# Optimization experiments

Measured on AMD Instinct MI355X. Metric: run time of the kernel, lower is better.

The kernel has to match this reference:

```python
import jax, jax.numpy as jnp
import numpy as np

HEADS = 4
DIM_HEAD = 32
SCALE = DIM_HEAD ** -0.5

# Energy conventions (Hopfield / Lagrangian formulation):
#  Neuron(x): g = activation(x); e = sum(x*g) - L(x)
#  Synapse(g, x): e = -sum(g*x)
#  identity Lagrangian: L(x) = 0.5*sum(x^2), g = x  => Conv2d block energy = -0.5*sum(x^2)
#  softmax Lagrangian: L(x) = sum(logsumexp(x, -1)), g = softmax(x, -1)

def setup_inputs() -> dict:
    key = jax.random.key(0)
    ks = jax.random.split(key, 5)
    b, c, h, w = 8, 256, 48, 48
    hidden = HEADS * DIM_HEAD  # 128
    return {
        "x": jax.random.normal(ks[0], (b, c, h, w), jnp.float32),
        "w_qkv": jax.random.normal(ks[1], (hidden * 3, c), jnp.float32) * 0.02,
        "b_qkv": jax.random.normal(ks[2], (hidden * 3,), jnp.float32) * 0.02,
        "w_out": jax.random.normal(ks[3], (c, hidden), jnp.float32) * 0.02,
        "b_out": jax.random.normal(ks[4], (c,), jnp.float32) * 0.02,
    }

def reference(x, w_qkv, b_qkv, w_out, b_out):
    b, c, h, w = x.shape
    # 1x1 conv == channel matmul
    qkv = jnp.einsum('oc,bcxy->boxy', w_qkv, x) + b_qkv[None, :, None, None]
    e_qkv = -0.5 * jnp.sum(qkv * qkv)  # identity-Lagrangian neuron + synapse energy
    q, k, v = jnp.split(qkv, 3, axis=1)
    # 'b (h c) x y -> b h c (x y)'
    def heads(t):
        return t.reshape(b, HEADS, DIM_HEAD, h * w)
    q, k, v = heads(q), heads(k), heads(v)
    q = q * SCALE
    sim = jnp.einsum('bhdi,bhdj->bhij', q, k)  # [b, heads, hw, hw]
    sim = sim - jax.lax.stop_gradient(jnp.max(sim, axis=-1, keepdims=True))
    attn = jax.nn.softmax(sim, axis=-1)
    # softmax-Lagrangian neuron energy: sum(sim*attn) - sum(logsumexp(sim, -1))
    e_attn = jnp.sum(sim * attn) - jnp.sum(jax.nn.logsumexp(sim, axis=-1))
    out = jnp.einsum('bhij,bhdj->bhid', attn, v)  # [b, heads, hw, dim_head]
    # 'b h (x y) d -> b (h d) x y'
    out = out.transpose(0, 1, 3, 2).reshape(b, HEADS * DIM_HEAD, h, w)
    out = jnp.einsum('oc,bcxy->boxy', w_out, out) + b_out[None, :, None, None]
    e_out = -0.5 * jnp.sum(out * out)
    return out, e_attn + e_out + e_qkv
```

## Files before the change

### kernel.cpp

```cpp
#include <hip/hip_runtime.h>
#include <hip/hip_bf16.h>

#define HW 2304
#define NB 8
#define NC 256
#define HID 128
#define DH 32
#define NH 4
#define SCALE 0.17677669529663687f
#define LOG2E 1.4426950408889634f
#define LN2   0.6931471805599453f

using bf16x8 = __attribute__((ext_vector_type(8))) short;
using f32x4  = __attribute__((ext_vector_type(4))) float;

__device__ __forceinline__ short f2bf(float f) {
    unsigned u = __float_as_uint(f);
    u += 0x7FFF + ((u >> 16) & 1);
    return (short)(u >> 16);
}
__device__ __forceinline__ unsigned pk2bf(float a, float b) {
    union { __hip_bfloat162 h; unsigned u; } cv;
    cv.h = __float22bfloat162_rn(float2{a, b});
    return cv.u;
}
__device__ __forceinline__ void gld16(const void* g, void* l) {
    __builtin_amdgcn_global_load_lds(
        (const __attribute__((address_space(1))) unsigned*)g,
        (__attribute__((address_space(3))) unsigned*)l, 16, 0, 0);
}

__global__ __launch_bounds__(256)
void prep(const float* __restrict__ x, const float* __restrict__ wq,
          const float* __restrict__ wo, short* __restrict__ Xt,
          short* __restrict__ Wq, short* __restrict__ Wo, float* __restrict__ wsz)
{
    if (blockIdx.z == 8) {
        const int bid = blockIdx.x + 72 * blockIdx.y;
        if (bid == 0 && threadIdx.x == 0) { wsz[0] = 0.f; ((int*)wsz)[1] = 0; }
        const int i = bid * 256 + threadIdx.x;
        if (i < 384 * 256) Wq[i] = f2bf(wq[i]);
        if (i < 256 * 128) Wo[i] = f2bf(wo[i]);
        return;
    }
    __shared__ float T[32][33];
    const int b = blockIdx.z, c0 = blockIdx.y * 32, s0 = blockIdx.x * 32;
    const int ts = threadIdx.x & 31, tc = threadIdx.x >> 5;
    #pragma unroll
    for (int cc = tc; cc < 32; cc += 8)
        T[cc][ts] = x[((size_t)b * NC + c0 + cc) * HW + s0 + ts];
    __syncthreads();
    const int tcc = threadIdx.x & 31, tss = threadIdx.x >> 5;
    #pragma unroll
    for (int ss = tss; ss < 32; ss += 8)
        Xt[((size_t)b * HW + s0 + ss) * NC + c0 + tcc] = f2bf(T[tcc][ss]);
}

template<int KD, bool QKV>
__global__ __launch_bounds__(256, 4)
void conv_mfma(const short* __restrict__ A, const short* __restrict__ Bt,
               const float* __restrict__ bias, float* __restrict__ out0,
               short* __restrict__ Qb, short* __restrict__ Kb,
               short* __restrict__ Vb, float* __restrict__ E,
               int* __restrict__ ticket, int nblocks, float* __restrict__ edst)
{
    const int b  = blockIdx.z;
    const int bm = blockIdx.y * 64;
    const int bn = blockIdx.x * 128;
    const int t  = threadIdx.x;
    const int w  = t >> 6, lane = t & 63;
    const int n16 = lane & 15, quad = lane >> 4;

    __shared__ __align__(16) char csm[24576];
    __shared__ float red[4];

    const int rL = lane >> 2, cswz = (lane & 3) ^ (rL & 3);
    const char* agl = (const char*)(A  + (size_t)(bm + rL) * KD + cswz * 8);
    const char* bgl = (const char*)(Bt + ((size_t)b * HW + bn + rL) * KD + cswz * 8);

    auto issue = [&](int kc, int pbuf) {
        char* base = csm + pbuf * 12288;
        if (w == 0) {
            gld16(agl + (size_t)(0 * 16 * KD + kc) * 2, base + 0 * 1024);
            gld16(agl + (size_t)(1 * 16 * KD + kc) * 2, base + 1 * 1024);
            gld16(bgl + (size_t)(0 * 16 * KD + kc) * 2, base + 4096 + 0 * 1024);
        } else if (w == 1) {
            gld16(agl + (size_t)(2 * 16 * KD + kc) * 2, base + 2 * 1024);
            gld16(agl + (size_t)(3 * 16 * KD + kc) * 2, base + 3 * 1024);
            gld16(bgl + (size_t)(1 * 16 * KD + kc) * 2, base + 4096 + 1 * 1024);
        } else if (w == 2) {
            gld16(bgl + (size_t)(2 * 16 * KD + kc) * 2, base + 4096 + 2 * 1024);
            gld16(bgl + (size_t)(3 * 16 * KD + kc) * 2, base + 4096 + 3 * 1024);
            gld16(bgl + (size_t)(4 * 16 * KD + kc) * 2, base + 4096 + 4 * 1024);
        } else {
            gld16(bgl + (size_t)(5 * 16 * KD + kc) * 2, base + 4096 + 5 * 1024);
            gld16(bgl + (size_t)(6 * 16 * KD + kc) * 2, base + 4096 + 6 * 1024);
            gld16(bgl + (size_t)(7 * 16 * KD + kc) * 2, base + 4096 + 7 * 1024);
        }
    };

    f32x4 acc[4][2] = {};
    const int rsw = (quad ^ (n16 & 3)) * 16;
    constexpr int NI = KD / 32;

    issue(0, 0);
    for (int ki = 0; ki < NI; ++ki) {
        const int p = ki & 1;
        __syncthreads();
        if (ki + 1 < NI) issue((ki + 1) * 32, p ^ 1);

        const char* Ap = csm + p * 12288;
        const char* Bp = Ap + 4096;
        bf16x8 am[4], bq[2];
        #pragma unroll
        for (int tm = 0; tm < 4; ++tm)
            am[tm] = *(const bf16x8*)(Ap + tm * 1024 + n16 * 64 + rsw);
        #pragma unroll
        for (int j = 0; j < 2; ++j)
            bq[j] = *(const bf16x8*)(Bp + (w * 2 + j) * 1024 + n16 * 64 + rsw);
        #pragma unroll
        for (int tm = 0; tm < 4; ++tm)
            #pragma unroll
            for (int j = 0; j < 2; ++j)
                acc[tm][j] = __builtin_amdgcn_mfma_f32_16x16x32_bf16(am[tm], bq[j], acc[tm][j], 0, 0, 0);
    }

    float e = 0.f;
    #pragma unroll
    for (int tm = 0; tm < 4; ++tm) {
        const int o0 = bm + tm * 16 + quad * 4;
        const float4 bb = *(const float4*)(bias + o0);
        #pragma unroll
        for (int j = 0; j < 2; ++j) {
            const int s = bn + (w * 2 + j) * 16 + n16;
            float v[4] = {acc[tm][j][0] + bb.x, acc[tm][j][1] + bb.y,
                          acc[tm][j][2] + bb.z, acc[tm][j][3] + bb.w};
            e -= 0.5f * (v[0]*v[0] + v[1]*v[1] + v[2]*v[2] + v[3]*v[3]);
            if (QKV) {
                if (o0 < HID) {
                    const int h = o0 >> 5, dh0 = o0 & 31;
                    const float qs = SCALE * LOG2E;
                    short4 pk = {f2bf(v[0]*qs), f2bf(v[1]*qs),
                                 f2bf(v[2]*qs), f2bf(v[3]*qs)};
                    *(short4*)(Qb + ((size_t)(b * NH + h) * HW + s) * DH + dh0) = pk;
                } else if (o0 < 2 * HID) {
                    const int c = o0 - HID, h = c >> 5, dh0 = c & 31;
                    const int g = s & 31;
                    const int sp = (s & ~31) | ((g & 4) << 2) | ((g >> 3) << 2) | (g & 3);
                    short4 pk = {f2bf(v[0]), f2bf(v[1]), f2bf(v[2]), f2bf(v[3])};
                    *(short4*)(Kb + ((size_t)(b * NH + h) * HW + sp) * DH + dh0) = pk;
                } else {
                    const int c = o0 - 2 * HID, h = c >> 5, dh0 = c & 31;
                    #pragma unroll
                    for (int r = 0; r < 4; ++r)
                        Vb[((size_t)(b * NH + h) * DH + dh0 + r) * HW + s] = f2bf(v[r]);
                }
            } else {
                #pragma unroll
                for (int r = 0; r < 4; ++r)
                    out0[((size_t)b * NC + o0 + r) * HW + s] = v[r];
            }
        }
    }

    #pragma unroll
    for (int off = 32; off > 0; off >>= 1) e += __shfl_down(e, off);
    if (lane == 0) red[w] = e;
    __syncthreads();
    if (t == 0) {
        atomicAdd(E, red[0] + red[1] + red[2] + red[3]);
        if (!QKV) {
            __threadfence();
            const int prev = atomicAdd(ticket, 1);
            if (prev == nblocks - 1) {
                __threadfence();
                edst[0] = atomicAdd(E, 0.f);
            }
        }
    }
}

__global__ __launch_bounds__(256)
void flash9(const short* __restrict__ Qb, const short* __restrict__ Kb,
            const short* __restrict__ Vb, short* __restrict__ attT,
            float* __restrict__ E)
{
    __shared__ __align__(16) char smem[16384];

    const int bh   = blockIdx.y;
    const int w    = threadIdx.x >> 6;
    const int lane = threadIdx.x & 63;
    const int n16  = lane & 15, quad = lane >> 4;
    const int qb   = blockIdx.x * 128 + w * 32;

    bf16x8 aq[2];
    #pragma unroll
    for (int qg = 0; qg < 2; ++qg)
        aq[qg] = *(const bf16x8*)(Qb + ((size_t)bh * HW + qb + qg * 16 + n16) * DH + quad * 8);

    const int rL = lane >> 2, cL = (lane & 3) ^ (rL & 3);
    const char* gbase; size_t gstep;
    if (w < 2) {
        gbase = (const char*)(Kb + (size_t)bh * HW * DH) + ((w & 1) * 16 + rL) * 64 + cL * 16;
        gstep = 2048;
    } else {
        gbase = (const char*)(Vb + (size_t)bh * DH * HW)
              + (size_t)((w & 1) * 16 + rL) * (HW * 2) + cL * 16;
        gstep = 64;
    }

    gld16(gbase,         smem + 0    + w * 1024);
    gld16(gbase + gstep, smem + 4096 + w * 1024);

    f32x4 acc[2][2] = {};
    float ls[2] = {}, ts[2] = {};
    const int swz = (quad ^ (n16 & 3)) * 8;

    for (int it = 0; it < 36; ++it) {
        const int p = it & 1;
        __syncthreads();
        if (it + 1 < 36) {
            const size_t g0 = (size_t)(2 * it + 2) * gstep;
            gld16(gbase + g0,         smem + (p ^ 1) * 8192 + 0    + w * 1024);
            gld16(gbase + g0 + gstep, smem + (p ^ 1) * 8192 + 4096 + w * 1024);
        }

        #pragma unroll
        for (int ca = 0; ca < 2; ++ca) {
            const short* kb = (const short*)(smem + p * 8192 + ca * 4096);

            const bf16x8 bk0 = *(const bf16x8*)(kb + n16 * 32 + swz);
            const bf16x8 bk1 = *(const bf16x8*)(kb + 512  + n16 * 32 + swz);
            const bf16x8 bv0 = *(const bf16x8*)(kb + 1024 + n16 * 32 + swz);
            const bf16x8 bv1 = *(const bf16x8*)(kb + 1536 + n16 * 32 + swz);

            #pragma unroll
            for (int qg = 0; qg < 2; ++qg) {
                f32x4 z = {};
                const f32x4 s0 = __builtin_amdgcn_mfma_f32_16x16x32_bf16(bk0, aq[qg], z, 0, 0, 0);
                const f32x4 s1 = __builtin_amdgcn_mfma_f32_16x16x32_bf16(bk1, aq[qg], z, 0, 0, 0);
                float e0[4], e1[4];
                #pragma unroll
                for (int r = 0; r < 4; ++r) {
                    e0[r] = __builtin_amdgcn_exp2f(s0[r]);
                    e1[r] = __builtin_amdgcn_exp2f(s1[r]);
                }
                ls[qg] += (e0[0] + e0[1]) + (e0[2] + e0[3])
                        + (e1[0] + e1[1]) + (e1[2] + e1[3]);
                ts[qg] += (e0[0]*s0[0] + e0[1]*s0[1]) + (e0[2]*s0[2] + e0[3]*s0[3])
                        + (e1[0]*s1[0] + e1[1]*s1[1]) + (e1[2]*s1[2] + e1[3]*s1[3]);
                union { bf16x8 v; unsigned u[4]; } pa;
                pa.u[0] = pk2bf(e0[0], e0[1]);
                pa.u[1] = pk2bf(e0[2], e0[3]);
                pa.u[2] = pk2bf(e1[0], e1[1]);
                pa.u[3] = pk2bf(e1[2], e1[3]);
                acc[qg][0] = __builtin_amdgcn_mfma_f32_16x16x32_bf16(bv0, pa.v, acc[qg][0], 0, 0, 0);
                acc[qg][1] = __builtin_amdgcn_mfma_f32_16x16x32_bf16(bv1, pa.v, acc[qg][1], 0, 0, 0);
            }
        }
    }

    #pragma unroll
    for (int qg = 0; qg < 2; ++qg) {
        ls[qg] += __shfl_xor(ls[qg], 16);
        ls[qg] += __shfl_xor(ls[qg], 32);
        ts[qg] += __shfl_xor(ts[qg], 16);
        ts[qg] += __shfl_xor(ts[qg], 32);
    }

    const int bb = bh >> 2, h = bh & 3;
    float e = 0.f;
    #pragma unroll
    for (int qg = 0; qg < 2; ++qg) {
        const int q = qb + qg * 16 + n16;
        const float L = ls[qg];
        const float invl = 1.f / L;
        short* ap = attT + ((size_t)bb * HW + q) * HID + h * 32;
        short4 pk0 = {f2bf(acc[qg][0][0] * invl), f2bf(acc[qg][0][1] * invl),
                      f2bf(acc[qg][0][2] * invl), f2bf(acc[qg][0][3] * invl)};
        short4 pk1 = {f2bf(acc[qg][1][0] * invl), f2bf(acc[qg][1][1] * invl),
                      f2bf(acc[qg][1][2] * invl), f2bf(acc[qg][1][3] * invl)};
        *(short4*)(ap + quad * 4)      = pk0;
        *(short4*)(ap + 16 + quad * 4) = pk1;
        if (quad == 0) e += (LN2 * ts[qg]) * invl - __logf(L);
    }
    #pragma unroll
    for (int m = 1; m < 64; m <<= 1) e += __shfl_xor(e, m);
    if (lane == 0) atomicAdd(E, e);
}

extern "C" void kernel_launch(void* const* d_in, const int* in_sizes, int n_in,
                              void* d_out, int out_size, void* d_ws, size_t ws_size,
                              hipStream_t stream) {
    const float* x     = (const float*)d_in[0];
    const float* w_qkv = (const float*)d_in[1];
    const float* b_qkv = (const float*)d_in[2];
    const float* w_out = (const float*)d_in[3];
    const float* b_out = (const float*)d_in[4];
    float* out = (float*)d_out;

    float* wsf    = (float*)d_ws;
    float* E      = wsf;
    int*   ticket = (int*)d_ws + 1;
    short* Xt   = (short*)(wsf + 16);
    short* Wq   = Xt + (size_t)NB * HW * NC;
    short* Wo   = Wq + 384 * 256;
    short* Qb   = Wo + 256 * 128;
    short* Kb   = Qb + (size_t)NB * NH * HW * DH;
    short* Vb   = Kb + (size_t)NB * NH * HW * DH;
    short* attT = Vb + (size_t)NB * NH * HW * DH;

    prep<<<dim3(HW / 32, NC / 32, NB + 1), 256, 0, stream>>>(
        x, w_qkv, w_out, Xt, Wq, Wo, wsf);
    conv_mfma<NC, true><<<dim3(18, 6, NB), 256, 0, stream>>>(
        Wq, Xt, b_qkv, nullptr, Qb, Kb, Vb, E, nullptr, 0, nullptr);
    flash9<<<dim3(HW / 128, NB * NH), 256, 0, stream>>>(
        Qb, Kb, Vb, attT, E);
    conv_mfma<HID, false><<<dim3(18, 4, NB), 256, 0, stream>>>(
        Wo, attT, b_out, out, nullptr, nullptr, nullptr, E,
        ticket, 18 * 4 * NB, out + (size_t)NB * NC * HW);
}
```

Measured before the change: 208.1 us.

## Split attention key range in two and merge partials in a combine kernel

The flash attention kernel now handles half of the key/value sequence per block, with a new grid z dimension of 2. This doubles the block count and is meant to improve CU utilisation and tail behaviour. Each half writes normalised bf16 partial outputs plus its row sums and energy terms. A new combine kernel weights the two partials by their row sums, writes the merged output and accumulates the softmax energy. The cost is an extra launch, extra global traffic for the partial outputs, and a second bf16 rounding of intermediate results.

New measurement: 207.8 us. About the same (-0.2%).

```diff
diff --git a/kernel.cpp b/kernel.cpp
--- a/kernel.cpp
+++ b/kernel.cpp
@@ -18,6 +18,9 @@
     unsigned u = __float_as_uint(f);
     u += 0x7FFF + ((u >> 16) & 1);
     return (short)(u >> 16);
+}
+__device__ __forceinline__ float bf2f(short s) {
+    return __uint_as_float(((unsigned)(unsigned short)s) << 16);
 }
 __device__ __forceinline__ unsigned pk2bf(float a, float b) {
     union { __hip_bfloat162 h; unsigned u; } cv;
@@ -181,13 +184,15 @@
 }
 
 __global__ __launch_bounds__(256)
-void flash9(const short* __restrict__ Qb, const short* __restrict__ Kb,
-            const short* __restrict__ Vb, short* __restrict__ attT,
-            float* __restrict__ E)
+void flashsplit(const short* __restrict__ Qb, const short* __restrict__ Kb,
+                const short* __restrict__ Vb, short* __restrict__ Oh0,
+                short* __restrict__ Oh1, float* __restrict__ lsP,
+                float* __restrict__ tsP)
 {
     __shared__ __align__(16) char smem[16384];
 
     const int bh   = blockIdx.y;
+    const int kh   = blockIdx.z;
     const int w    = threadIdx.x >> 6;
     const int lane = threadIdx.x & 63;
     const int n16  = lane & 15, quad = lane >> 4;
@@ -208,6 +213,7 @@
               + (size_t)((w & 1) * 16 + rL) * (HW * 2) + cL * 16;
         gstep = 64;
     }
+    gbase += (size_t)kh * 36 * gstep;
 
     gld16(gbase,         smem + 0    + w * 1024);
     gld16(gbase + gstep, smem + 4096 + w * 1024);
@@ -216,10 +222,10 @@
     float ls[2] = {}, ts[2] = {};
     const int swz = (quad ^ (n16 & 3)) * 8;
 
-    for (int it = 0; it < 36; ++it) {
+    for (int it = 0; it < 18; ++it) {
         const int p = it & 1;
         __syncthreads();
-        if (it + 1 < 36) {
+        if (it + 1 < 18) {
             const size_t g0 = (size_t)(2 * it + 2) * gstep;
             gld16(gbase + g0,         smem + (p ^ 1) * 8192 + 0    + w * 1024);
             gld16(gbase + g0 + gstep, smem + (p ^ 1) * 8192 + 4096 + w * 1024);
@@ -269,24 +275,62 @@
     }
 
     const int bb = bh >> 2, h = bh & 3;
-    float e = 0.f;
+    short* dst = kh ? Oh1 : Oh0;
     #pragma unroll
     for (int qg = 0; qg < 2; ++qg) {
         const int q = qb + qg * 16 + n16;
         const float L = ls[qg];
         const float invl = 1.f / L;
-        short* ap = attT + ((size_t)bb * HW + q) * HID + h * 32;
+        short* ap = dst + ((size_t)bb * HW + q) * HID + h * 32;
         short4 pk0 = {f2bf(acc[qg][0][0] * invl), f2bf(acc[qg][0][1] * invl),
                       f2bf(acc[qg][0][2] * invl), f2bf(acc[qg][0][3] * invl)};
         short4 pk1 = {f2bf(acc[qg][1][0] * invl), f2bf(acc[qg][1][1] * invl),
                       f2bf(acc[qg][1][2] * invl), f2bf(acc[qg][1][3] * invl)};
         *(short4*)(ap + quad * 4)      = pk0;
         *(short4*)(ap + 16 + quad * 4) = pk1;
-        if (quad == 0) e += (LN2 * ts[qg]) * invl - __logf(L);
-    }
-    #pragma unroll
-    for (int m = 1; m < 64; m <<= 1) e += __shfl_xor(e, m);
-    if (lane == 0) atomicAdd(E, e);
+        if (quad == 0) {
+            const size_t li = (size_t)(kh * 32 + bh) * HW + q;
+            lsP[li] = L;
+            tsP[li] = ts[qg];
+        }
+    }
+}
+
+__global__ __launch_bounds__(256)
+void combine(short* __restrict__ attT, const short* __restrict__ Oh1,
+             const float* __restrict__ lsP, const float* __restrict__ tsP,
+             float* __restrict__ E)
+{
+    __shared__ float red[4];
+    const int bh = blockIdx.y, b = bh >> 2, h = bh & 3;
+    const int t = threadIdx.x;
+    const int q = blockIdx.x * 64 + (t >> 2);
+    const int dg = (t & 3) * 8;
+    const size_t l0 = (size_t)bh * HW + q;
+    const size_t l1 = (size_t)(32 + bh) * HW + q;
+    const float L0 = lsP[l0], L1 = lsP[l1];
+    const float L = L0 + L1;
+    const float w0 = L0 / L, w1 = L1 / L;
+
+    short* ap = attT + ((size_t)b * HW + q) * HID + h * 32 + dg;
+    const short* bp = Oh1 + ((size_t)b * HW + q) * HID + h * 32 + dg;
+    const bf16x8 o0 = *(const bf16x8*)ap;
+    const bf16x8 o1 = *(const bf16x8*)bp;
+    union { bf16x8 v; unsigned u[4]; } pk;
+    #pragma unroll
+    for (int i = 0; i < 4; ++i)
+        pk.u[i] = pk2bf(w0 * bf2f(o0[2*i])     + w1 * bf2f(o1[2*i]),
+                        w0 * bf2f(o0[2*i + 1]) + w1 * bf2f(o1[2*i + 1]));
+    *(bf16x8*)ap = pk.v;
+
+    float e = 0.f;
+    if ((t & 3) == 0)
+        e = (LN2 * (tsP[l0] + tsP[l1])) / L - __logf(L);
+    #pragma unroll
+    for (int off = 32; off > 0; off >>= 1) e += __shfl_down(e, off);
+    if ((t & 63) == 0) red[t >> 6] = e;
+    __syncthreads();
+    if (t == 0) atomicAdd(E, red[0] + red[1] + red[2] + red[3]);
 }
 
 extern "C" void kernel_launch(void* const* d_in, const int* in_sizes, int n_in,
@@ -309,13 +353,18 @@
     short* Kb   = Qb + (size_t)NB * NH * HW * DH;
     short* Vb   = Kb + (size_t)NB * NH * HW * DH;
     short* attT = Vb + (size_t)NB * NH * HW * DH;
+    short* attT2= attT + (size_t)NB * HW * HID;
+    float* lsP  = (float*)(attT2 + (size_t)NB * HW * HID);
+    float* tsP  = lsP + 2 * 32 * HW;
 
     prep<<<dim3(HW / 32, NC / 32, NB + 1), 256, 0, stream>>>(
         x, w_qkv, w_out, Xt, Wq, Wo, wsf);
     conv_mfma<NC, true><<<dim3(18, 6, NB), 256, 0, stream>>>(
         Wq, Xt, b_qkv, nullptr, Qb, Kb, Vb, E, nullptr, 0, nullptr);
-    flash9<<<dim3(HW / 128, NB * NH), 256, 0, stream>>>(
-        Qb, Kb, Vb, attT, E);
+    flashsplit<<<dim3(18, NB * NH, 2), 256, 0, stream>>>(
+        Qb, Kb, Vb, attT, attT2, lsP, tsP);
+    combine<<<dim3(HW / 64, NB * NH), 256, 0, stream>>>(
+        attT, attT2, lsP, tsP, E);
     conv_mfma<HID, false><<<dim3(18, 4, NB), 256, 0, stream>>>(
         Wo, attT, b_out, out, nullptr, nullptr, nullptr, E,
         ticket, 18 * 4 * NB, out + (size_t)NB * NC * HW);
```

## Split attention over key dimension and merge partials inside output projection

Applied to the files above, without the earlier changes.

The flash attention kernel now splits the key/value range into four chunks via a third grid dimension, raising the block count from 576 to 2304 to fill more CUs. Each chunk writes normalized partial outputs in bf16 plus per-row sum and entropy terms. The output 1x1 conv kernel merges these partials, weighted by their sums, while staging its B operand, and also computes the attention energy term. This adds extra global traffic for four partial outputs and rounds each partial to bf16. The combine relies on all splits sharing a fixed max, which holds because the logits are not max-subtracted.

Result: faster. 196.3 us (-5.7%).

```diff
diff --git a/kernel.cpp b/kernel.cpp
--- a/kernel.cpp
+++ b/kernel.cpp
@@ -11,6 +11,9 @@
 #define LOG2E 1.4426950408889634f
 #define LN2   0.6931471805599453f
 
+#define NSPLIT 4
+#define OSZ ((size_t)NB * HW * HID)
+
 using bf16x8 = __attribute__((ext_vector_type(8))) short;
 using f32x4  = __attribute__((ext_vector_type(4))) float;
 
@@ -18,6 +21,9 @@
     unsigned u = __float_as_uint(f);
     u += 0x7FFF + ((u >> 16) & 1);
     return (short)(u >> 16);
+}
+__device__ __forceinline__ float bf2f(short s) {
+    return __uint_as_float(((unsigned)(unsigned short)s) << 16);
 }
 __device__ __forceinline__ unsigned pk2bf(float a, float b) {
     union { __hip_bfloat162 h; unsigned u; } cv;
@@ -56,14 +62,13 @@
         Xt[((size_t)b * HW + s0 + ss) * NC + c0 + tcc] = f2bf(T[tcc][ss]);
 }
 
-template<int KD, bool QKV>
 __global__ __launch_bounds__(256, 4)
-void conv_mfma(const short* __restrict__ A, const short* __restrict__ Bt,
-               const float* __restrict__ bias, float* __restrict__ out0,
-               short* __restrict__ Qb, short* __restrict__ Kb,
-               short* __restrict__ Vb, float* __restrict__ E,
-               int* __restrict__ ticket, int nblocks, float* __restrict__ edst)
+void conv_qkv(const short* __restrict__ A, const short* __restrict__ Bt,
+              const float* __restrict__ bias,
+              short* __restrict__ Qb, short* __restrict__ Kb,
+              short* __restrict__ Vb, float* __restrict__ E)
 {
+    constexpr int KD = NC;
     const int b  = blockIdx.z;
     const int bm = blockIdx.y * 64;
     const int bn = blockIdx.x * 128;
@@ -136,29 +141,23 @@
             float v[4] = {acc[tm][j][0] + bb.x, acc[tm][j][1] + bb.y,
                           acc[tm][j][2] + bb.z, acc[tm][j][3] + bb.w};
             e -= 0.5f * (v[0]*v[0] + v[1]*v[1] + v[2]*v[2] + v[3]*v[3]);
-            if (QKV) {
-                if (o0 < HID) {
-                    const int h = o0 >> 5, dh0 = o0 & 31;
-                    const float qs = SCALE * LOG2E;
-                    short4 pk = {f2bf(v[0]*qs), f2bf(v[1]*qs),
-                                 f2bf(v[2]*qs), f2bf(v[3]*qs)};
-                    *(short4*)(Qb + ((size_t)(b * NH + h) * HW + s) * DH + dh0) = pk;
-                } else if (o0 < 2 * HID) {
-                    const int c = o0 - HID, h = c >> 5, dh0 = c & 31;
-                    const int g = s & 31;
-                    const int sp = (s & ~31) | ((g & 4) << 2) | ((g >> 3) << 2) | (g & 3);
-                    short4 pk = {f2bf(v[0]), f2bf(v[1]), f2bf(v[2]), f2bf(v[3])};
-                    *(short4*)(Kb + ((size_t)(b * NH + h) * HW + sp) * DH + dh0) = pk;
-                } else {
-                    const int c = o0 - 2 * HID, h = c >> 5, dh0 = c & 31;
-                    #pragma unroll
-                    for (int r = 0; r < 4; ++r)
-                        Vb[((size_t)(b * NH + h) * DH + dh0 + r) * HW + s] = f2bf(v[r]);
-                }
+            if (o0 < HID) {
+                const int h = o0 >> 5, dh0 = o0 & 31;
+                const float qs = SCALE * LOG2E;
+                short4 pk = {f2bf(v[0]*qs), f2bf(v[1]*qs),
+                             f2bf(v[2]*qs), f2bf(v[3]*qs)};
+                *(short4*)(Qb + ((size_t)(b * NH + h) * HW + s) * DH + dh0) = pk;
+            } else if (o0 < 2 * HID) {
+                const int c = o0 - HID, h = c >> 5, dh0 = c & 31;
+                const int g = s & 31;
+                const int sp = (s & ~31) | ((g & 4) << 2) | ((g >> 3) << 2) | (g & 3);
+                short4 pk = {f2bf(v[0]), f2bf(v[1]), f2bf(v[2]), f2bf(v[3])};
+                *(short4*)(Kb + ((size_t)(b * NH + h) * HW + sp) * DH + dh0) = pk;
             } else {
+                const int c = o0 - 2 * HID, h = c >> 5, dh0 = c & 31;
                 #pragma unroll
                 for (int r = 0; r < 4; ++r)
-                    out0[((size_t)b * NC + o0 + r) * HW + s] = v[r];
+                    Vb[((size_t)(b * NH + h) * DH + dh0 + r) * HW + s] = f2bf(v[r]);
             }
         }
     }
@@ -167,27 +166,19 @@
     for (int off = 32; off > 0; off >>= 1) e += __shfl_down(e, off);
     if (lane == 0) red[w] = e;
     __syncthreads();
-    if (t == 0) {
-        atomicAdd(E, red[0] + red[1] + red[2] + red[3]);
-        if (!QKV) {
-            __threadfence();
-            const int prev = atomicAdd(ticket, 1);
-            if (prev == nblocks - 1) {
-                __threadfence();
-                edst[0] = atomicAdd(E, 0.f);
-            }
-        }
-    }
+    if (t == 0) atomicAdd(E, red[0] + red[1] + red[2] + red[3]);
 }
 
 __global__ __launch_bounds__(256)
-void flash9(const short* __restrict__ Qb, const short* __restrict__ Kb,
-            const short* __restrict__ Vb, short* __restrict__ attT,
-            float* __restrict__ E)
+void flashsplit(const short* __restrict__ Qb, const short* __restrict__ Kb,
+                const short* __restrict__ Vb, short* __restrict__ Oh,
+                float* __restrict__ lsP, float* __restrict__ tsP)
 {
     __shared__ __align__(16) char smem[16384];
 
+    constexpr int ITERS = HW / (NSPLIT * 64);
     const int bh   = blockIdx.y;
+    const int kh   = blockIdx.z;
     const int w    = threadIdx.x >> 6;
     const int lane = threadIdx.x & 63;
     const int n16  = lane & 15, quad = lane >> 4;
@@ -208,6 +199,7 @@
               + (size_t)((w & 1) * 16 + rL) * (HW * 2) + cL * 16;
         gstep = 64;
     }
+    gbase += (size_t)kh * (2 * ITERS) * gstep;
 
     gld16(gbase,         smem + 0    + w * 1024);
     gld16(gbase + gstep, smem + 4096 + w * 1024);
@@ -216,10 +208,10 @@
     float ls[2] = {}, ts[2] = {};
     const int swz = (quad ^ (n16 & 3)) * 8;
 
-    for (int it = 0; it < 36; ++it) {
+    for (int it = 0; it < ITERS; ++it) {
         const int p = it & 1;
         __syncthreads();
-        if (it + 1 < 36) {
+        if (it + 1 < ITERS) {
             const size_t g0 = (size_t)(2 * it + 2) * gstep;
             gld16(gbase + g0,         smem + (p ^ 1) * 8192 + 0    + w * 1024);
             gld16(gbase + g0 + gstep, smem + (p ^ 1) * 8192 + 4096 + w * 1024);
@@ -269,24 +261,174 @@
     }
 
     const int bb = bh >> 2, h = bh & 3;
-    float e = 0.f;
+    short* dst = Oh + (size_t)kh * OSZ;
     #pragma unroll
     for (int qg = 0; qg < 2; ++qg) {
         const int q = qb + qg * 16 + n16;
         const float L = ls[qg];
         const float invl = 1.f / L;
-        short* ap = attT + ((size_t)bb * HW + q) * HID + h * 32;
+        short* ap = dst + ((size_t)bb * HW + q) * HID + h * 32;
         short4 pk0 = {f2bf(acc[qg][0][0] * invl), f2bf(acc[qg][0][1] * invl),
                       f2bf(acc[qg][0][2] * invl), f2bf(acc[qg][0][3] * invl)};
         short4 pk1 = {f2bf(acc[qg][1][0] * invl), f2bf(acc[qg][1][1] * invl),
                       f2bf(acc[qg][1][2] * invl), f2bf(acc[qg][1][3] * invl)};
         *(short4*)(ap + quad * 4)      = pk0;
         *(short4*)(ap + 16 + quad * 4) = pk1;
-        if (quad == 0) e += (LN2 * ts[qg]) * invl - __logf(L);
-    }
-    #pragma unroll
-    for (int m = 1; m < 64; m <<= 1) e += __shfl_xor(e, m);
-    if (lane == 0) atomicAdd(E, e);
+        if (quad == 0) {
+            const size_t li = (size_t)(kh * 32 + bh) * HW + q;
+            lsP[li] = L;
+            tsP[li] = ts[qg];
+        }
+    }
+}
+
+__global__ __launch_bounds__(256, 2)
+void conv_out(const short* __restrict__ A, const short* __restrict__ Oh,
+              const float* __restrict__ lsP, const float* __restrict__ tsP,
+              const float* __restrict__ bias, float* __restrict__ out0,
+              float* __restrict__ E, int* __restrict__ ticket, int nblocks,
+              float* __restrict__ edst)
+{
+    constexpr int KD = HID;
+    constexpr int NI = KD / 32;
+    const int b  = blockIdx.z;
+    const int bm = blockIdx.y * 64;
+    const int bn = blockIdx.x * 128;
+    const int t  = threadIdx.x;
+    const int w  = t >> 6, lane = t & 63;
+    const int n16 = lane & 15, quad = lane >> 4;
+
+    __shared__ __align__(16) char csm[24576];
+    __shared__ float red[4];
+
+    const int rL = lane >> 2, cswz = (lane & 3) ^ (rL & 3);
+    const char* agl = (const char*)(A + (size_t)(bm + rL) * KD + cswz * 8);
+
+    auto issueA = [&](int kc, int pbuf) {
+        char* base = csm + pbuf * 12288;
+        if (w == 0) {
+            gld16(agl + (size_t)(0 * 16 * KD + kc) * 2, base + 0 * 1024);
+            gld16(agl + (size_t)(1 * 16 * KD + kc) * 2, base + 1 * 1024);
+        } else if (w == 1) {
+            gld16(agl + (size_t)(2 * 16 * KD + kc) * 2, base + 2 * 1024);
+            gld16(agl + (size_t)(3 * 16 * KD + kc) * 2, base + 3 * 1024);
+        }
+    };
+
+    auto loadB = [&](int ki, bf16x8 pk[2]) {
+        const int kc = ki * 32;
+        const int bh = b * NH + ki;
+        #pragma unroll
+        for (int d = 0; d < 2; ++d) {
+            const int blk = w * 2 + d;
+            const int q = bn + blk * 16 + rL;
+            float Ls[NSPLIT], sum = 0.f;
+            #pragma unroll
+            for (int kh = 0; kh < NSPLIT; ++kh) {
+                Ls[kh] = lsP[(size_t)(kh * 32 + bh) * HW + q];
+                sum += Ls[kh];
+            }
+            const float inv = 1.f / sum;
+            float vv[8] = {};
+            #pragma unroll
+            for (int kh = 0; kh < NSPLIT; ++kh) {
+                const float wk = Ls[kh] * inv;
+                const bf16x8 o = *(const bf16x8*)(Oh + (size_t)kh * OSZ
+                                    + ((size_t)b * HW + q) * HID + kc + cswz * 8);
+                #pragma unroll
+                for (int j = 0; j < 8; ++j) vv[j] += wk * bf2f(o[j]);
+            }
+            union { bf16x8 v; unsigned u[4]; } c;
+            #pragma unroll
+            for (int i = 0; i < 4; ++i) c.u[i] = pk2bf(vv[2*i], vv[2*i+1]);
+            pk[d] = c.v;
+        }
+    };
+    auto writeB = [&](const bf16x8 pk[2], int pbuf) {
+        char* base = csm + pbuf * 12288 + 4096;
+        #pragma unroll
+        for (int d = 0; d < 2; ++d) {
+            const int blk = w * 2 + d;
+            *(bf16x8*)(base + blk * 1024 + rL * 64 + (lane & 3) * 16) = pk[d];
+        }
+    };
+
+    f32x4 acc[4][2] = {};
+    const int rsw = (quad ^ (n16 & 3)) * 16;
+
+    bf16x8 bpk[2];
+    loadB(0, bpk);
+    issueA(0, 0);
+    writeB(bpk, 0);
+    for (int ki = 0; ki < NI; ++ki) {
+        const int p = ki & 1;
+        __syncthreads();
+        if (ki + 1 < NI) { loadB(ki + 1, bpk); issueA((ki + 1) * 32, p ^ 1); }
+
+        const char* Ap = csm + p * 12288;
+        const char* Bp = Ap + 4096;
+        bf16x8 am[4], bq[2];
+        #pragma unroll
+        for (int tm = 0; tm < 4; ++tm)
+            am[tm] = *(const bf16x8*)(Ap + tm * 1024 + n16 * 64 + rsw);
+        #pragma unroll
+        for (int j = 0; j < 2; ++j)
+            bq[j] = *(const bf16x8*)(Bp + (w * 2 + j) * 1024 + n16 * 64 + rsw);
+        #pragma unroll
+        for (int tm = 0; tm < 4; ++tm)
+            #pragma unroll
+            for (int j = 0; j < 2; ++j)
+                acc[tm][j] = __builtin_amdgcn_mfma_f32_16x16x32_bf16(am[tm], bq[j], acc[tm][j], 0, 0, 0);
+
+        if (ki + 1 < NI) writeB(bpk, p ^ 1);
+    }
+
+    float e = 0.f;
+    #pragma unroll
+    for (int tm = 0; tm < 4; ++tm) {
+        const int o0 = bm + tm * 16 + quad * 4;
+        const float4 bb = *(const float4*)(bias + o0);
+        #pragma unroll
+        for (int j = 0; j < 2; ++j) {
+            const int s = bn + (w * 2 + j) * 16 + n16;
+            float v[4] = {acc[tm][j][0] + bb.x, acc[tm][j][1] + bb.y,
+                          acc[tm][j][2] + bb.z, acc[tm][j][3] + bb.w};
+            e -= 0.5f * (v[0]*v[0] + v[1]*v[1] + v[2]*v[2] + v[3]*v[3]);
+            #pragma unroll
+            for (int r = 0; r < 4; ++r)
+                out0[((size_t)b * NC + o0 + r) * HW + s] = v[r];
+        }
+    }
+
+    if (blockIdx.y == 0) {
+        const int q = bn + (t & 127);
+        #pragma unroll
+        for (int jj = 0; jj < 2; ++jj) {
+            const int h = (t >> 7) * 2 + jj;
+            const int bh = b * NH + h;
+            float L = 0.f, T = 0.f;
+            #pragma unroll
+            for (int kh = 0; kh < NSPLIT; ++kh) {
+                L += lsP[(size_t)(kh * 32 + bh) * HW + q];
+                T += tsP[(size_t)(kh * 32 + bh) * HW + q];
+            }
+            e += (LN2 * T) / L - __logf(L);
+        }
+    }
+
+    #pragma unroll
+    for (int off = 32; off > 0; off >>= 1) e += __shfl_down(e, off);
+    if (lane == 0) red[w] = e;
+    __syncthreads();
+    if (t == 0) {
+        atomicAdd(E, red[0] + red[1] + red[2] + red[3]);
+        __threadfence();
+        const int prev = atomicAdd(ticket, 1);
+        if (prev == nblocks - 1) {
+            __threadfence();
+            edst[0] = atomicAdd(E, 0.f);
+        }
+    }
 }
 
 extern "C" void kernel_launch(void* const* d_in, const int* in_sizes, int n_in,
@@ -308,15 +450,17 @@
     short* Qb   = Wo + 256 * 128;
     short* Kb   = Qb + (size_t)NB * NH * HW * DH;
     short* Vb   = Kb + (size_t)NB * NH * HW * DH;
-    short* attT = Vb + (size_t)NB * NH * HW * DH;
+    short* Oh   = Vb + (size_t)NB * NH * HW * DH;
+    float* lsP  = (float*)(Oh + NSPLIT * OSZ);
+    float* tsP  = lsP + NSPLIT * 32 * HW;
 
     prep<<<dim3(HW / 32, NC / 32, NB + 1), 256, 0, stream>>>(
         x, w_qkv, w_out, Xt, Wq, Wo, wsf);
-    conv_mfma<NC, true><<<dim3(18, 6, NB), 256, 0, stream>>>(
-        Wq, Xt, b_qkv, nullptr, Qb, Kb, Vb, E, nullptr, 0, nullptr);
-    flash9<<<dim3(HW / 128, NB * NH), 256, 0, stream>>>(
-        Qb, Kb, Vb, attT, E);
-    conv_mfma<HID, false><<<dim3(18, 4, NB), 256, 0, stream>>>(
-        Wo, attT, b_out, out, nullptr, nullptr, nullptr, E,
-        ticket, 18 * 4 * NB, out + (size_t)NB * NC * HW);
-}
+    conv_qkv<<<dim3(18, 6, NB), 256, 0, stream>>>(
+        Wq, Xt, b_qkv, Qb, Kb, Vb, E);
+    flashsplit<<<dim3(HW / 128, NB * NH, NSPLIT), 256, 0, stream>>>(
+        Qb, Kb, Vb, Oh, lsP, tsP);
+    conv_out<<<dim3(18, 4, NB), 256, 0, stream>>>(
+        Wo, Oh, lsP, tsP, b_out, out, E, ticket, 18 * 4 * NB,
+        out + (size_t)NB * NC * HW);
+}
```
